# Performance work log

Measured on AMD Instinct MI355X. Metric: run time of the kernel, lower is better.

The kernel has to match this reference:

```python
import jax, jax.numpy as jnp
import numpy as np

B, S, D, FF, E = 4, 2048, 2048, 8192, 2


def setup_inputs() -> dict:
    key = jax.random.key(0)
    k0, k1, k2, k3, k4 = jax.random.split(key, 5)
    s = 0.02  # init scale for weights
    return {
        "hidden_states": jax.random.normal(k0, (B, S, D), jnp.float32),
        "gate_w": jax.random.normal(k1, (E, D), jnp.float32) * s,   # router Linear weight
        "w_gate": jax.random.normal(k2, (E, FF, D), jnp.float32) * s,  # per-expert gate_proj
        "w_up": jax.random.normal(k3, (E, FF, D), jnp.float32) * s,    # per-expert up_proj
        "w_down": jax.random.normal(k4, (E, D, FF), jnp.float32) * s,  # per-expert down_proj
    }


def reference(hidden_states, gate_w, w_gate, w_up, w_down):
    b, s, d = hidden_states.shape
    x = hidden_states.reshape(-1, d)                      # [T, D], T = B*S
    logits = x @ gate_w.T                                  # [T, E]
    probs = jax.nn.softmax(logits.astype(jnp.float32), axis=-1)
    sel = jnp.argmax(probs, axis=-1)                       # top-1 expert per token
    top_w = jnp.take_along_axis(probs, sel[:, None], axis=-1)  # [T, 1] routing weight
    onehot = jax.nn.one_hot(sel, gate_w.shape[0], dtype=x.dtype)  # [T, E]
    # Dense per-expert MistralMLP: down(silu(gate(x)) * up(x)); top-1 combine via one-hot mask.
    g = jnp.einsum('td,efd->etf', x, w_gate)               # [E, T, FF]
    u = jnp.einsum('td,efd->etf', x, w_up)                 # [E, T, FF]
    h = jax.nn.silu(g) * u
    y = jnp.einsum('etf,edf->etd', h, w_down)              # [E, T, D]
    out = jnp.einsum('etd,te->td', y, onehot * top_w)      # weighted scatter-combine
    return out.reshape(b, s, d)
```

## Files before the change

### kernel.cpp

```cpp
#include <hip/hip_runtime.h>
#include <hip/hip_bf16.h>

#define T_TOK   8192
#define D_DIM   2048
#define FF_DIM  8192
#define PADT    8448
#define NMT     33
#define G1_GRID (NMT*64)
#define G2_GRID (NMT*8)
#define NT1     64
#define NT2     256

#define C_CNT0 0
#define C_CNT1 1
#define C_CUR0 2
#define C_BASE1 4
#define C_PTOT 5

typedef __attribute__((ext_vector_type(4))) float f32x4;
typedef __attribute__((ext_vector_type(8))) short short8;

__device__ __forceinline__ unsigned short f2bf(float f) {
  union { __hip_bfloat16 b; unsigned short u; } cv;
  cv.b = __float2bfloat16(f);
  return cv.u;
}

__device__ __forceinline__ void gload16(const void* g, void* l) {
  __builtin_amdgcn_global_load_lds(
      (const __attribute__((address_space(1))) void*)g,
      (__attribute__((address_space(3))) void*)l,
      16, 0, 0);
}

__global__ __launch_bounds__(256) void cvt3_kernel(const float4* __restrict__ sa,
                                                   const float4* __restrict__ sb,
                                                   const float4* __restrict__ sc,
                                                   ushort4* __restrict__ da,
                                                   ushort4* __restrict__ db,
                                                   ushort4* __restrict__ dc, int n4) {
  const int stride = gridDim.x * blockDim.x;
  for (int i = blockIdx.x * blockDim.x + threadIdx.x; i < n4; i += stride) {
    float4 v = sa[i];
    da[i] = make_ushort4(f2bf(v.x), f2bf(v.y), f2bf(v.z), f2bf(v.w));
    v = sb[i];
    db[i] = make_ushort4(f2bf(v.x), f2bf(v.y), f2bf(v.z), f2bf(v.w));
    v = sc[i];
    dc[i] = make_ushort4(f2bf(v.x), f2bf(v.y), f2bf(v.z), f2bf(v.w));
  }
}

__global__ __launch_bounds__(256) void init_kernel(int* __restrict__ ctrl,
                                                   int* __restrict__ perm) {
  int i = blockIdx.x * blockDim.x + threadIdx.x;
  if (i < 8) ctrl[i] = 0;
  if (i < PADT) perm[i] = -1;
}

__global__ __launch_bounds__(256) void router_kernel(const float* __restrict__ x,
                                                     const float* __restrict__ gw,
                                                     int* __restrict__ sel,
                                                     float* __restrict__ topw,
                                                     int* __restrict__ ctrl) {
  const int w = threadIdx.x >> 6, l = threadIdx.x & 63;
  const int t = blockIdx.x * 4 + w;
  const float4* xr = (const float4*)(x + (size_t)t * D_DIM);
  const float4* g0 = (const float4*)gw;
  const float4* g1 = (const float4*)(gw + D_DIM);
  float d0 = 0.f, d1 = 0.f;
#pragma unroll
  for (int i = 0; i < 8; i++) {
    float4 v = xr[i * 64 + l];
    float4 a = g0[i * 64 + l];
    float4 b = g1[i * 64 + l];
    d0 += v.x * a.x + v.y * a.y + v.z * a.z + v.w * a.w;
    d1 += v.x * b.x + v.y * b.y + v.z * b.z + v.w * b.w;
  }
#pragma unroll
  for (int s = 32; s; s >>= 1) {
    d0 += __shfl_xor(d0, s);
    d1 += __shfl_xor(d1, s);
  }
  if (l == 0) {
    int e = (d1 > d0) ? 1 : 0;
    float dd = fabsf(d1 - d0);
    sel[t] = e;
    topw[t] = 1.f / (1.f + expf(-dd));
    atomicAdd(&ctrl[e], 1);
  }
}

__global__ void setup_kernel(int* __restrict__ ctrl) {
  if (threadIdx.x == 0) {
    int c0 = ctrl[C_CNT0], c1 = ctrl[C_CNT1];
    int b1 = ((c0 + 255) >> 8) << 8;
    ctrl[C_BASE1] = b1;
    ctrl[C_PTOT] = b1 + (((c1 + 255) >> 8) << 8);
  }
}

__global__ __launch_bounds__(256) void scatter_kernel(const int* __restrict__ sel,
                                                      int* __restrict__ ctrl,
                                                      int* __restrict__ perm) {
  int t = blockIdx.x * blockDim.x + threadIdx.x;
  int e = sel[t];
  int base = e ? ctrl[C_BASE1] : 0;
  int pos = base + atomicAdd(&ctrl[C_CUR0 + e], 1);
  perm[pos] = t;
}

__global__ __launch_bounds__(256) void gather_kernel(const float* __restrict__ x,
                                                     const int* __restrict__ perm,
                                                     const float* __restrict__ topw,
                                                     ushort* __restrict__ Xg,
                                                     float* __restrict__ twg) {
  const int w = threadIdx.x >> 6, l = threadIdx.x & 63;
  const int pos = blockIdx.x * 4 + w;
  const int t = perm[pos];
  if (l == 0) twg[pos] = (t >= 0) ? topw[t] : 0.f;
  ushort4* dst = (ushort4*)(Xg + (size_t)pos * D_DIM);
  if (t >= 0) {
    const float4* src = (const float4*)(x + (size_t)t * D_DIM);
#pragma unroll
    for (int i = 0; i < 8; i++) {
      float4 v = src[i * 64 + l];
      dst[i * 64 + l] = make_ushort4(f2bf(v.x), f2bf(v.y), f2bf(v.z), f2bf(v.w));
    }
  } else {
    ushort4 z = make_ushort4(0, 0, 0, 0);
#pragma unroll
    for (int i = 0; i < 8; i++) dst[i * 64 + l] = z;
  }
}


__global__ __launch_bounds__(512, 2) void gemm1_kernel(const ushort* __restrict__ Xg,
                                                       const ushort* __restrict__ Wg,
                                                       const ushort* __restrict__ Wu,
                                                       ushort* __restrict__ H,
                                                       const int* __restrict__ ctrl) {
  __shared__ ushort lds[3 * 16384];
  const int ptot = ctrl[C_PTOT];
  const int bid = blockIdx.x;
  const int swz = (bid & 7) * (G1_GRID / 8) + (bid >> 3);
  const int tn = swz / NMT, bx = swz % NMT;
  const int row0 = bx * 256;
  if (row0 >= ptot) return;
  const int e = (row0 >= ctrl[C_BASE1]) ? 1 : 0;

  const int tid = threadIdx.x, w = tid >> 6, l = tid & 63;
  const int wr = w >> 2, wc = w & 3;
  const int fr = l & 15, kg = l >> 4;

  auto srcptr = [&](int li) -> const ushort* {
    int o = li * 8192 + w * 1024 + l * 16;
    int row = o >> 7, pc = (o >> 4) & 7;
    int lc = pc ^ (row & 7);
    if (lc < 4)
      return Xg + (size_t)(row0 + row) * D_DIM + lc * 8;
    int mat = (row >> 4) & 1;
    int ff = tn * 128 + ((row >> 5) << 4) + (row & 15);
    return (mat ? Wu : Wg) + ((size_t)e * FF_DIM + ff) * D_DIM + (lc - 4) * 8;
  };
  const ushort* s0 = srcptr(0);
  const ushort* s1 = srcptr(1);
  const ushort* s2 = srcptr(2);
  const ushort* s3 = srcptr(3);

  auto STAGE = [&](int buf) {
    ushort* db = lds + buf * 16384 + (w << 9);
    gload16(s0, db);          s0 += 32;
    gload16(s1, db + 4096);   s1 += 32;
    gload16(s2, db + 8192);   s2 += 32;
    gload16(s3, db + 12288);  s3 += 32;
  };

  const int aoff = (wr * 128 + fr) * 128 + ((kg ^ (fr & 7)) << 4);
  const int boff = (wc * 64 + fr) * 128 + (((4 ^ kg) ^ (fr & 7)) << 4);

  f32x4 acc[8][4] = {};

  STAGE(0);
  STAGE(1);
  int sbuf = 2, cbuf = 0;
  for (int t = 0; t < NT1; ++t) {
    if (t < NT1 - 1) asm volatile("s_waitcnt vmcnt(4)" ::: "memory");
    else             asm volatile("s_waitcnt vmcnt(0)" ::: "memory");
    __builtin_amdgcn_s_barrier();
    asm volatile("" ::: "memory");
    if (t + 2 < NT1) {
      STAGE(sbuf);
      sbuf = (sbuf == 2) ? 0 : sbuf + 1;
    }
    const char* Lb = (const char*)lds + cbuf * 32768;
    cbuf = (cbuf == 2) ? 0 : cbuf + 1;
    short8 bfrag[4], afrag[8];
#pragma unroll
    for (int j = 0; j < 4; j++) bfrag[j] = *(const short8*)(Lb + boff + j * 2048);
#pragma unroll
    for (int i = 0; i < 8; i++) afrag[i] = *(const short8*)(Lb + aoff + i * 2048);
    __builtin_amdgcn_s_setprio(1);
#pragma unroll
    for (int i = 0; i < 8; i++)
#pragma unroll
      for (int j = 0; j < 4; j++)
        acc[i][j] = __builtin_amdgcn_mfma_f32_16x16x32_bf16(afrag[i], bfrag[j], acc[i][j], 0, 0, 0);
    __builtin_amdgcn_s_setprio(0);
    asm volatile("" ::: "memory");
  }

  const int m4 = kg * 4;
#pragma unroll
  for (int i = 0; i < 8; i++) {
#pragma unroll
    for (int r = 0; r < 4; r++) {
      size_t hbase = (size_t)(row0 + wr * 128 + i * 16 + m4 + r) * FF_DIM;
#pragma unroll
      for (int p = 0; p < 2; p++) {
        float g = acc[i][2 * p][r], u = acc[i][2 * p + 1][r];
        float h = (g / (1.f + __expf(-g))) * u;
        H[hbase + tn * 128 + (wc * 2 + p) * 16 + fr] = f2bf(h);
      }
    }
  }
}

__global__ __launch_bounds__(512, 2) void gemm2_kernel(const ushort* __restrict__ Hb,
                                                       const ushort* __restrict__ Wd,
                                                       const int* __restrict__ perm,
                                                       const float* __restrict__ twg,
                                                       float* __restrict__ out,
                                                       const int* __restrict__ ctrl) {
  __shared__ ushort lds[3 * 16384];
  const int ptot = ctrl[C_PTOT];
  const int bid = blockIdx.x;
  const int swz = (bid & 7) * (G2_GRID / 8) + (bid >> 3);
  const int tn = swz / NMT, bx = swz % NMT;
  const int row0 = bx * 256;
  if (row0 >= ptot) return;
  const int e = (row0 >= ctrl[C_BASE1]) ? 1 : 0;

  const int tid = threadIdx.x, w = tid >> 6, l = tid & 63;
  const int wr = w >> 2, wc = w & 3;
  const int fr = l & 15, kg = l >> 4;

  auto srcptr = [&](int li) -> const ushort* {
    int o = li * 8192 + w * 1024 + l * 16;
    int row = o >> 7, pc = (o >> 4) & 7;
    int lc = pc ^ (row & 7);
    if (lc < 4)
      return Hb + (size_t)(row0 + row) * FF_DIM + lc * 8;
    return Wd + ((size_t)e * D_DIM + tn * 256 + row) * FF_DIM + (lc - 4) * 8;
  };
  const ushort* s0 = srcptr(0);
  const ushort* s1 = srcptr(1);
  const ushort* s2 = srcptr(2);
  const ushort* s3 = srcptr(3);

  auto STAGE = [&](int buf) {
    ushort* db = lds + buf * 16384 + (w << 9);
    gload16(s0, db);          s0 += 32;
    gload16(s1, db + 4096);   s1 += 32;
    gload16(s2, db + 8192);   s2 += 32;
    gload16(s3, db + 12288);  s3 += 32;
  };

  const int aoff = (wr * 128 + fr) * 128 + ((kg ^ (fr & 7)) << 4);
  const int boff = (wc * 64 + fr) * 128 + (((4 ^ kg) ^ (fr & 7)) << 4);

  f32x4 acc[8][4] = {};

  STAGE(0);
  STAGE(1);
  int sbuf = 2, cbuf = 0;
  for (int t = 0; t < NT2; ++t) {
    if (t < NT2 - 1) asm volatile("s_waitcnt vmcnt(4)" ::: "memory");
    else             asm volatile("s_waitcnt vmcnt(0)" ::: "memory");
    __builtin_amdgcn_s_barrier();
    asm volatile("" ::: "memory");
    if (t + 2 < NT2) {
      STAGE(sbuf);
      sbuf = (sbuf == 2) ? 0 : sbuf + 1;
    }
    const char* Lb = (const char*)lds + cbuf * 32768;
    cbuf = (cbuf == 2) ? 0 : cbuf + 1;
    short8 bfrag[4], afrag[8];
#pragma unroll
    for (int j = 0; j < 4; j++) bfrag[j] = *(const short8*)(Lb + boff + j * 2048);
#pragma unroll
    for (int i = 0; i < 8; i++) afrag[i] = *(const short8*)(Lb + aoff + i * 2048);
    __builtin_amdgcn_s_setprio(1);
#pragma unroll
    for (int i = 0; i < 8; i++)
#pragma unroll
      for (int j = 0; j < 4; j++)
        acc[i][j] = __builtin_amdgcn_mfma_f32_16x16x32_bf16(afrag[i], bfrag[j], acc[i][j], 0, 0, 0);
    __builtin_amdgcn_s_setprio(0);
    asm volatile("" ::: "memory");
  }

  const int m4 = kg * 4;
#pragma unroll
  for (int i = 0; i < 8; i++) {
#pragma unroll
    for (int r = 0; r < 4; r++) {
      int prow = row0 + wr * 128 + i * 16 + m4 + r;
      int tok = perm[prow];
      if (tok < 0) continue;
      float tw = twg[prow];
      float* orow = out + (size_t)tok * D_DIM + tn * 256 + wc * 64;
#pragma unroll
      for (int j = 0; j < 4; j++) orow[j * 16 + fr] = acc[i][j][r] * tw;
    }
  }
}

extern "C" void kernel_launch(void* const* d_in, const int* in_sizes, int n_in,
                              void* d_out, int out_size, void* d_ws, size_t ws_size,
                              hipStream_t stream) {
  const float* x  = (const float*)d_in[0];
  const float* gw = (const float*)d_in[1];
  const float* wg = (const float*)d_in[2];
  const float* wu = (const float*)d_in[3];
  const float* wd = (const float*)d_in[4];
  float* out = (float*)d_out;

  char* ws = (char*)d_ws;
  size_t off = 0;
  auto alloc = [&](size_t bytes) -> void* {
    void* p = ws + off;
    off += (bytes + 255) & ~(size_t)255;
    return p;
  };
  const size_t WELEM = (size_t)2 * FF_DIM * D_DIM;
  ushort* Wg_b = (ushort*)alloc(WELEM * 2);
  ushort* Wu_b = (ushort*)alloc(WELEM * 2);
  ushort* Wd_b = (ushort*)alloc(WELEM * 2);
  ushort* Xg   = (ushort*)alloc((size_t)PADT * D_DIM * 2);
  ushort* Hbuf = (ushort*)alloc((size_t)PADT * FF_DIM * 2);
  int*   sel  = (int*)alloc(T_TOK * 4);
  float* topw = (float*)alloc(T_TOK * 4);
  int*   perm = (int*)alloc(PADT * 4);
  float* twg  = (float*)alloc(PADT * 4);
  int*   ctrl = (int*)alloc(256);
  (void)ws_size; (void)in_sizes; (void)n_in; (void)out_size;

  const int n4 = (int)(WELEM / 4);
  cvt3_kernel<<<4096, 256, 0, stream>>>((const float4*)wg, (const float4*)wu,
                                        (const float4*)wd, (ushort4*)Wg_b,
                                        (ushort4*)Wu_b, (ushort4*)Wd_b, n4);

  init_kernel<<<(PADT + 255) / 256, 256, 0, stream>>>(ctrl, perm);
  router_kernel<<<T_TOK / 4, 256, 0, stream>>>(x, gw, sel, topw, ctrl);
  setup_kernel<<<1, 64, 0, stream>>>(ctrl);
  scatter_kernel<<<T_TOK / 256, 256, 0, stream>>>(sel, ctrl, perm);
  gather_kernel<<<PADT / 4, 256, 0, stream>>>(x, perm, topw, Xg, twg);

  gemm1_kernel<<<G1_GRID, 512, 0, stream>>>(Xg, Wg_b, Wu_b, Hbuf, ctrl);
  gemm2_kernel<<<G2_GRID, 512, 0, stream>>>(Hbuf, Wd_b, perm, twg, out, ctrl);
}
```

Before: 1.649 ms.

## Split-K the down-projection GEMM with atomic accumulation and interleave loads in both GEMMs

The down-projection GEMM grid was only 33x8 blocks, so it now splits the FF reduction four ways, and each split adds its partial sums into a pre-zeroed output with float atomics. A zeroing kernel is added to clear the output first. Both GEMM main loops now issue the next-stage global-to-LDS loads in two halves, interleaved with two halves of the MFMA work behind extra barriers, to spread memory traffic across the compute. The trade is more atomics, an extra full pass over the output, more barriers per iteration, and a non-deterministic summation order.

Measured after the change: 1.701 ms. +3.1%, slower.

```diff
diff --git a/kernel.cpp b/kernel.cpp
--- a/kernel.cpp
+++ b/kernel.cpp
@@ -7,9 +7,10 @@
 #define PADT    8448
 #define NMT     33
 #define G1_GRID (NMT*64)
-#define G2_GRID (NMT*8)
+#define KSPLIT  4
+#define G2_GRID (NMT*8*KSPLIT)
 #define NT1     64
-#define NT2     256
+#define NT2     64
 
 #define C_CNT0 0
 #define C_CNT1 1
@@ -50,6 +51,12 @@
   }
 }
 
+__global__ __launch_bounds__(256) void zero_out_kernel(float4* __restrict__ o, int n4) {
+  const int stride = gridDim.x * blockDim.x;
+  for (int i = blockIdx.x * blockDim.x + threadIdx.x; i < n4; i += stride)
+    o[i] = make_float4(0.f, 0.f, 0.f, 0.f);
+}
+
 __global__ __launch_bounds__(256) void init_kernel(int* __restrict__ ctrl,
                                                    int* __restrict__ perm) {
   int i = blockIdx.x * blockDim.x + threadIdx.x;
@@ -188,23 +195,45 @@
     else             asm volatile("s_waitcnt vmcnt(0)" ::: "memory");
     __builtin_amdgcn_s_barrier();
     asm volatile("" ::: "memory");
-    if (t + 2 < NT1) {
-      STAGE(sbuf);
-      sbuf = (sbuf == 2) ? 0 : sbuf + 1;
-    }
     const char* Lb = (const char*)lds + cbuf * 32768;
     cbuf = (cbuf == 2) ? 0 : cbuf + 1;
-    short8 bfrag[4], afrag[8];
+    ushort* db = lds + sbuf * 16384 + (w << 9);
+    short8 bfrag[4], af0[4], af1[4];
 #pragma unroll
     for (int j = 0; j < 4; j++) bfrag[j] = *(const short8*)(Lb + boff + j * 2048);
 #pragma unroll
-    for (int i = 0; i < 8; i++) afrag[i] = *(const short8*)(Lb + aoff + i * 2048);
+    for (int i = 0; i < 4; i++) af0[i] = *(const short8*)(Lb + aoff + i * 2048);
+    if (t + 2 < NT1) {
+      gload16(s0, db);          s0 += 32;
+      gload16(s1, db + 4096);   s1 += 32;
+    }
+    __builtin_amdgcn_s_barrier();
+    asm volatile("" ::: "memory");
     __builtin_amdgcn_s_setprio(1);
 #pragma unroll
-    for (int i = 0; i < 8; i++)
+    for (int i = 0; i < 4; i++)
 #pragma unroll
       for (int j = 0; j < 4; j++)
-        acc[i][j] = __builtin_amdgcn_mfma_f32_16x16x32_bf16(afrag[i], bfrag[j], acc[i][j], 0, 0, 0);
+        acc[i][j] = __builtin_amdgcn_mfma_f32_16x16x32_bf16(af0[i], bfrag[j], acc[i][j], 0, 0, 0);
+    __builtin_amdgcn_s_setprio(0);
+    asm volatile("" ::: "memory");
+    __builtin_amdgcn_s_barrier();
+    asm volatile("" ::: "memory");
+#pragma unroll
+    for (int i = 0; i < 4; i++) af1[i] = *(const short8*)(Lb + aoff + (i + 4) * 2048);
+    if (t + 2 < NT1) {
+      gload16(s2, db + 8192);   s2 += 32;
+      gload16(s3, db + 12288);  s3 += 32;
+      sbuf = (sbuf == 2) ? 0 : sbuf + 1;
+    }
+    __builtin_amdgcn_s_barrier();
+    asm volatile("" ::: "memory");
+    __builtin_amdgcn_s_setprio(1);
+#pragma unroll
+    for (int i = 0; i < 4; i++)
+#pragma unroll
+      for (int j = 0; j < 4; j++)
+        acc[i + 4][j] = __builtin_amdgcn_mfma_f32_16x16x32_bf16(af1[i], bfrag[j], acc[i + 4][j], 0, 0, 0);
     __builtin_amdgcn_s_setprio(0);
     asm volatile("" ::: "memory");
   }
@@ -235,10 +264,13 @@
   const int ptot = ctrl[C_PTOT];
   const int bid = blockIdx.x;
   const int swz = (bid & 7) * (G2_GRID / 8) + (bid >> 3);
-  const int tn = swz / NMT, bx = swz % NMT;
+  const int ksl = swz / (NMT * 8);
+  const int rem = swz % (NMT * 8);
+  const int tn = rem / NMT, bx = rem % NMT;
   const int row0 = bx * 256;
   if (row0 >= ptot) return;
   const int e = (row0 >= ctrl[C_BASE1]) ? 1 : 0;
+  const int ks0 = ksl * (FF_DIM / KSPLIT);
 
   const int tid = threadIdx.x, w = tid >> 6, l = tid & 63;
   const int wr = w >> 2, wc = w & 3;
@@ -249,8 +281,8 @@
     int row = o >> 7, pc = (o >> 4) & 7;
     int lc = pc ^ (row & 7);
     if (lc < 4)
-      return Hb + (size_t)(row0 + row) * FF_DIM + lc * 8;
-    return Wd + ((size_t)e * D_DIM + tn * 256 + row) * FF_DIM + (lc - 4) * 8;
+      return Hb + (size_t)(row0 + row) * FF_DIM + ks0 + lc * 8;
+    return Wd + ((size_t)e * D_DIM + tn * 256 + row) * FF_DIM + ks0 + (lc - 4) * 8;
   };
   const ushort* s0 = srcptr(0);
   const ushort* s1 = srcptr(1);
@@ -278,23 +310,45 @@
     else             asm volatile("s_waitcnt vmcnt(0)" ::: "memory");
     __builtin_amdgcn_s_barrier();
     asm volatile("" ::: "memory");
-    if (t + 2 < NT2) {
-      STAGE(sbuf);
-      sbuf = (sbuf == 2) ? 0 : sbuf + 1;
-    }
     const char* Lb = (const char*)lds + cbuf * 32768;
     cbuf = (cbuf == 2) ? 0 : cbuf + 1;
-    short8 bfrag[4], afrag[8];
+    ushort* db = lds + sbuf * 16384 + (w << 9);
+    short8 bfrag[4], af0[4], af1[4];
 #pragma unroll
     for (int j = 0; j < 4; j++) bfrag[j] = *(const short8*)(Lb + boff + j * 2048);
 #pragma unroll
-    for (int i = 0; i < 8; i++) afrag[i] = *(const short8*)(Lb + aoff + i * 2048);
+    for (int i = 0; i < 4; i++) af0[i] = *(const short8*)(Lb + aoff + i * 2048);
+    if (t + 2 < NT2) {
+      gload16(s0, db);          s0 += 32;
+      gload16(s1, db + 4096);   s1 += 32;
+    }
+    __builtin_amdgcn_s_barrier();
+    asm volatile("" ::: "memory");
     __builtin_amdgcn_s_setprio(1);
 #pragma unroll
-    for (int i = 0; i < 8; i++)
+    for (int i = 0; i < 4; i++)
 #pragma unroll
       for (int j = 0; j < 4; j++)
-        acc[i][j] = __builtin_amdgcn_mfma_f32_16x16x32_bf16(afrag[i], bfrag[j], acc[i][j], 0, 0, 0);
+        acc[i][j] = __builtin_amdgcn_mfma_f32_16x16x32_bf16(af0[i], bfrag[j], acc[i][j], 0, 0, 0);
+    __builtin_amdgcn_s_setprio(0);
+    asm volatile("" ::: "memory");
+    __builtin_amdgcn_s_barrier();
+    asm volatile("" ::: "memory");
+#pragma unroll
+    for (int i = 0; i < 4; i++) af1[i] = *(const short8*)(Lb + aoff + (i + 4) * 2048);
+    if (t + 2 < NT2) {
+      gload16(s2, db + 8192);   s2 += 32;
+      gload16(s3, db + 12288);  s3 += 32;
+      sbuf = (sbuf == 2) ? 0 : sbuf + 1;
+    }
+    __builtin_amdgcn_s_barrier();
+    asm volatile("" ::: "memory");
+    __builtin_amdgcn_s_setprio(1);
+#pragma unroll
+    for (int i = 0; i < 4; i++)
+#pragma unroll
+      for (int j = 0; j < 4; j++)
+        acc[i + 4][j] = __builtin_amdgcn_mfma_f32_16x16x32_bf16(af1[i], bfrag[j], acc[i + 4][j], 0, 0, 0);
     __builtin_amdgcn_s_setprio(0);
     asm volatile("" ::: "memory");
   }
@@ -310,7 +364,7 @@
       float tw = twg[prow];
       float* orow = out + (size_t)tok * D_DIM + tn * 256 + wc * 64;
 #pragma unroll
-      for (int j = 0; j < 4; j++) orow[j * 16 + fr] = acc[i][j][r] * tw;
+      for (int j = 0; j < 4; j++) atomicAdd(&orow[j * 16 + fr], acc[i][j][r] * tw);
     }
   }
 }
@@ -349,6 +403,7 @@
   cvt3_kernel<<<4096, 256, 0, stream>>>((const float4*)wg, (const float4*)wu,
                                         (const float4*)wd, (ushort4*)Wg_b,
                                         (ushort4*)Wu_b, (ushort4*)Wd_b, n4);
+  zero_out_kernel<<<2048, 256, 0, stream>>>((float4*)out, T_TOK * D_DIM / 4);
 
   init_kernel<<<(PADT + 255) / 256, 256, 0, stream>>>(ctrl, perm);
   router_kernel<<<T_TOK / 4, 256, 0, stream>>>(x, gw, sel, topw, ctrl);
```
